# Kernel optimization log

Hardware: AMD Instinct MI355X
Metric: run time of the kernel (lower is better)

The kernel has to match this reference:

```python
import jax, jax.numpy as jnp
import numpy as np

N = 50000
E = 800000
IN_F = 128
HID = 128
OUT_F = 64
MU = 2.0
EPS = 1e-12


def setup_inputs() -> dict:
    key = jax.random.key(0)
    ks = jax.random.split(key, 20)
    d = {}
    d["x"] = jax.random.normal(ks[0], (N, IN_F), dtype=jnp.float32)
    d["edge_src"] = jax.random.randint(ks[1], (E,), 0, N, dtype=jnp.int32)
    d["edge_dst"] = jax.random.randint(ks[2], (E,), 0, N, dtype=jnp.int32)
    d["edge_val"] = jax.random.uniform(ks[3], (E,), dtype=jnp.float32)
    # layer 0: in=128 -> pool=128 -> out=128 (activation=relu)
    s0 = 1.0 / np.sqrt(IN_F)
    d["pool_w0"] = jax.random.uniform(ks[4], (IN_F, IN_F), jnp.float32, -s0, s0)
    d["pool_b0"] = jax.random.uniform(ks[5], (IN_F,), jnp.float32, -s0, s0)
    d["fc1_w0"] = jax.random.uniform(ks[6], (HID, IN_F), jnp.float32, -s0, s0)
    d["fc1_b0"] = jax.random.uniform(ks[7], (HID,), jnp.float32, -s0, s0)
    d["fc2_w0"] = jax.random.uniform(ks[8], (HID, IN_F), jnp.float32, -s0, s0)
    d["fc2_b0"] = jax.random.uniform(ks[9], (HID,), jnp.float32, -s0, s0)
    # layer 1 (final): in=128 -> pool=128 -> out=64 (no activation)
    s1 = 1.0 / np.sqrt(HID)
    d["pool_w1"] = jax.random.uniform(ks[10], (HID, HID), jnp.float32, -s1, s1)
    d["pool_b1"] = jax.random.uniform(ks[11], (HID,), jnp.float32, -s1, s1)
    d["fc1_w1"] = jax.random.uniform(ks[12], (OUT_F, HID), jnp.float32, -s1, s1)
    d["fc1_b1"] = jax.random.uniform(ks[13], (OUT_F,), jnp.float32, -s1, s1)
    d["fc2_w1"] = jax.random.uniform(ks[14], (OUT_F, HID), jnp.float32, -s1, s1)
    d["fc2_b1"] = jax.random.uniform(ks[15], (OUT_F,), jnp.float32, -s1, s1)
    return d


def _sage_conv(x, src, dst, val, pw, pb, w1, b1, w2, b2, act):
    # L2-normalize rows (F.normalize(x, dim=1))
    xn = x / jnp.maximum(jnp.linalg.norm(x, axis=1, keepdims=True), EPS)
    h = jax.nn.relu(xn @ pw.T + pb)               # [N, pool]
    h_mu = h ** MU                                # elementwise pow
    # spmm(adj, h_mu): gather source rows, scale by edge weight, scatter-add to dst rows
    agg = jax.ops.segment_sum(h_mu[src] * val[:, None], dst, num_segments=N)
    agg = agg ** (1.0 / MU)                       # generalized-mean root
    out = (h @ w1.T + b1) + (agg @ w2.T + b2)
    return jax.nn.relu(out) if act else out


def reference(x, edge_src, edge_dst, edge_val,
              pool_w0, pool_b0, fc1_w0, fc1_b0, fc2_w0, fc2_b0,
              pool_w1, pool_b1, fc1_w1, fc1_b1, fc2_w1, fc2_b1):
    h = _sage_conv(x, edge_src, edge_dst, edge_val,
                   pool_w0, pool_b0, fc1_w0, fc1_b0, fc2_w0, fc2_b0, act=True)
    out = _sage_conv(h, edge_src, edge_dst, edge_val,
                     pool_w1, pool_b1, fc1_w1, fc1_b1, fc2_w1, fc2_b1, act=False)
    return out
```

## Files before the change

### kernel.cpp

```cpp
#include <hip/hip_runtime.h>

#define FF 128
#define BCAP 8192
#define CHUNK 4096
#define PITCH 136
#define BSTRIDE 32
#define PBCACHE 6144

typedef __attribute__((ext_vector_type(8))) short short8;
typedef __attribute__((ext_vector_type(4))) float f32x4;

__device__ __forceinline__ unsigned short bf16_rne(float f) {
    unsigned u = __float_as_uint(f);
    u += 0x7fffu + ((u >> 16) & 1u);
    return (unsigned short)(u >> 16);
}
__device__ __forceinline__ float bf16_to_f32(unsigned short h) {
    return __uint_as_float(((unsigned)h) << 16);
}

__global__ __launch_bounds__(256, 2)
void poolpartA_kernel(const float* __restrict__ x,
                      const unsigned short* __restrict__ Wh, const unsigned short* __restrict__ Wl,
                      const float* __restrict__ bias,
                      unsigned short* __restrict__ hout,
                      const int* __restrict__ esrc, const int* __restrict__ edst,
                      const float* __restrict__ eval,
                      int* __restrict__ bucket_cnt, int2* __restrict__ ebuf,
                      int N, int E, int nchunks)
{
    __shared__ alignas(16) char smem[37888];
    const int t = threadIdx.x;

    if (blockIdx.x < nchunks) {
        int* cnt   = (int*)smem;
        int* sc    = cnt + 256;
        int* excl  = sc + 256;
        int* cur   = excl + 256;
        int* gbase = cur + 256;
        int2* staged = (int2*)(smem + 5 * 256 * 4);
        const int e0 = blockIdx.x * CHUNK;
        const int n  = min(CHUNK, E - e0);

        unsigned pk[16]; float vr[16];
        #pragma unroll
        for (int k = 0; k < 16; ++k) {
            const int i = t + k * 256;
            pk[k] = 0xFFFFFFFFu;
            if (i < n) {
                int d = edst[e0 + i];
                int s = esrc[e0 + i];
                pk[k] = (unsigned)((s & 0xffff) | (d << 16));
                vr[k] = eval[e0 + i];
            }
        }

        cnt[t] = 0;
        __syncthreads();
        #pragma unroll
        for (int k = 0; k < 16; ++k)
            if (pk[k] != 0xFFFFFFFFu) atomicAdd(&cnt[pk[k] >> 24], 1);
        __syncthreads();

        sc[t] = cnt[t];
        __syncthreads();
        #pragma unroll
        for (int off = 1; off < 256; off <<= 1) {
            int v = (t >= off) ? sc[t - off] : 0;
            __syncthreads();
            sc[t] += v;
            __syncthreads();
        }
        excl[t] = sc[t] - cnt[t];
        cur[t]  = excl[t];
        if (cnt[t] > 0) gbase[t] = atomicAdd(&bucket_cnt[t * BSTRIDE], cnt[t]);
        __syncthreads();

        #pragma unroll
        for (int k = 0; k < 16; ++k) {
            if (pk[k] != 0xFFFFFFFFu) {
                int b = pk[k] >> 24;
                int slot = atomicAdd(&cur[b], 1);
                staged[slot] = make_int2((int)pk[k], __float_as_int(vr[k]));
            }
        }
        __syncthreads();

        for (int p = t; p < n; p += 256) {
            int2 ent = staged[p];
            int b = ((unsigned)ent.x) >> 24;
            int gpos = gbase[b] + (p - excl[b]);
            ebuf[(size_t)b * BCAP + gpos] = ent;
        }
    } else {
        unsigned short* sX = (unsigned short*)smem;
        float* sNorm = (float*)(smem + 64 * PITCH * 2);
        const int tile = blockIdx.x - nchunks;

        const int lane = t & 63, wave = t >> 6;
        const int quad = lane >> 4, l16 = lane & 15;

        short8 Bh[2][4], Bl[2][4];
        #pragma unroll
        for (int c = 0; c < 2; ++c) {
            const int jt = 2 * wave + c;
            #pragma unroll
            for (int tt = 0; tt < 4; ++tt) {
                const size_t o = ((size_t)(jt * 4 + tt) * 64 + lane) * 8;
                Bh[c][tt] = *(const short8*)&Wh[o];
                Bl[c][tt] = *(const short8*)&Wl[o];
            }
        }

        #pragma unroll
        for (int rg = 0; rg < 2; ++rg) {
            const int row = rg * 32 + (t >> 3);
            const int c0  = (t & 7) * 16;
            const int n   = tile * 64 + row;
            const int base = row * PITCH + c0;
            float v[16];
            if (n < N) {
                const float4* p = (const float4*)(x + (size_t)n * FF + c0);
                #pragma unroll
                for (int i = 0; i < 4; ++i) {
                    float4 q = p[i];
                    v[4*i] = q.x; v[4*i+1] = q.y; v[4*i+2] = q.z; v[4*i+3] = q.w;
                }
            } else {
                #pragma unroll
                for (int i = 0; i < 16; ++i) v[i] = 0.f;
            }
            float ss = 0.f;
            #pragma unroll
            for (int i = 0; i < 16; ++i) ss = fmaf(v[i], v[i], ss);
            union { unsigned short u[8]; short8 s; } h0, h1;
            #pragma unroll
            for (int i = 0; i < 8; ++i) {
                h0.u[i] = bf16_rne(v[i]);
                h1.u[i] = bf16_rne(v[8 + i]);
            }
            *(short8*)&sX[base]     = h0.s;
            *(short8*)&sX[base + 8] = h1.s;
            ss += __shfl_xor(ss, 1);
            ss += __shfl_xor(ss, 2);
            ss += __shfl_xor(ss, 4);
            if ((t & 7) == 0) sNorm[row] = 1.0f / fmaxf(sqrtf(ss), 1e-12f);
        }
        __syncthreads();

        f32x4 acc[4][2];
        #pragma unroll
        for (int r = 0; r < 4; ++r)
            #pragma unroll
            for (int c = 0; c < 2; ++c) {
                f32x4 z = {0.f, 0.f, 0.f, 0.f};
                acc[r][c] = z;
            }

        #pragma unroll
        for (int tt = 0; tt < 4; ++tt) {
            short8 Ah[4];
            #pragma unroll
            for (int r = 0; r < 4; ++r)
                Ah[r] = *(const short8*)&sX[(r * 16 + l16) * PITCH + tt * 32 + quad * 8];
            #pragma unroll
            for (int c = 0; c < 2; ++c)
                #pragma unroll
                for (int r = 0; r < 4; ++r) {
                    acc[r][c] = __builtin_amdgcn_mfma_f32_16x16x32_bf16(Ah[r], Bh[c][tt], acc[r][c], 0, 0, 0);
                    acc[r][c] = __builtin_amdgcn_mfma_f32_16x16x32_bf16(Ah[r], Bl[c][tt], acc[r][c], 0, 0, 0);
                }
        }

        __syncthreads();
        #pragma unroll
        for (int c = 0; c < 2; ++c) {
            const int j = (2 * wave + c) * 16 + l16;
            const float bj = bias[j];
            #pragma unroll
            for (int r = 0; r < 4; ++r) {
                #pragma unroll
                for (int g = 0; g < 4; ++g) {
                    const int nl = r * 16 + quad * 4 + g;
                    float s = sNorm[nl];
                    float val = fmaf(acc[r][c][g], s, bj);
                    val = fmaxf(val, 0.f);
                    sX[nl * PITCH + j] = bf16_rne(val);
                }
            }
        }
        __syncthreads();
        #pragma unroll
        for (int rg = 0; rg < 2; ++rg) {
            const int row = rg * 32 + (t >> 3);
            const int c0  = (t & 7) * 16;
            const int n   = tile * 64 + row;
            if (n < N) {
                const int base = row * PITCH + c0;
                *(short8*)&hout[(size_t)n * FF + c0]     = *(short8*)&sX[base];
                *(short8*)&hout[(size_t)n * FF + c0 + 8] = *(short8*)&sX[base + 8];
            }
        }
    }
}

struct WPack {
    const float* src[6];
    unsigned short* hi[6];
    unsigned short* lo[6];
    int n[6];
};

__global__ __launch_bounds__(256)
void wprep_kernel(WPack p, int* __restrict__ bucket_cnt)
{
    if (blockIdx.x == 0) {
        for (int i = threadIdx.x; i < 256 * BSTRIDE; i += 256) bucket_cnt[i] = 0;
    }
    int id = blockIdx.x * 256 + threadIdx.x;
    #pragma unroll
    for (int i = 0; i < 6; ++i) {
        if (id < p.n[i]) {
            float f = p.src[i][id];
            unsigned short h = bf16_rne(f);
            const int j = id >> 7, k = id & 127;
            const int jt = j >> 4, l16 = j & 15;
            const int t = k >> 5, quad = (k >> 3) & 3, j8 = k & 7;
            const size_t o = ((size_t)((jt * 4 + t) * 4 + quad) * 16 + l16) * 8 + j8;
            p.hi[i][o] = h;
            p.lo[i][o] = bf16_rne(f - bf16_to_f32(h));
            return;
        }
        id -= p.n[i];
    }
}

__global__ __launch_bounds__(256)
void partB_kernel(const int* __restrict__ bucket_cnt, const int2* __restrict__ ebuf,
                  int* __restrict__ offsets, int2* __restrict__ edata,
                  int N, int E, int nbuck)
{
    __shared__ int pre[256], hist[256], sc[256], excl[256], cur[256];
    __shared__ int2 sBuf[PBCACHE];
    const int t = threadIdx.x;
    const int b = blockIdx.x;

    const int cnt_self = bucket_cnt[b * BSTRIDE];
    const int2* ib = ebuf + (size_t)b * BCAP;
    const bool useL = (cnt_self <= PBCACHE);

    if (useL)
        for (int i = t; i < cnt_self; i += 256) sBuf[i] = ib[i];

    pre[t] = (t < nbuck) ? bucket_cnt[t * BSTRIDE] : 0;
    hist[t] = 0;
    __syncthreads();
    #pragma unroll
    for (int off = 1; off < 256; off <<= 1) {
        int v = (t >= off) ? pre[t - off] : 0;
        __syncthreads();
        pre[t] += v;
        __syncthreads();
    }
    const int base = (b == 0) ? 0 : pre[b - 1];
    const int cnt  = cnt_self;

    for (int i = t; i < cnt; i += 256) {
        int2 ent = useL ? sBuf[i] : ib[i];
        atomicAdd(&hist[(((unsigned)ent.x) >> 16) & 255], 1);
    }
    __syncthreads();

    sc[t] = hist[t];
    __syncthreads();
    #pragma unroll
    for (int off = 1; off < 256; off <<= 1) {
        int v = (t >= off) ? sc[t - off] : 0;
        __syncthreads();
        sc[t] += v;
        __syncthreads();
    }
    excl[t] = sc[t] - hist[t];
    cur[t]  = excl[t];

    const int node = b * 256 + t;
    if (node <= N) offsets[node] = base + excl[t];
    __syncthreads();

    for (int i = t; i < cnt; i += 256) {
        int2 ent = useL ? sBuf[i] : ib[i];
        int l = (((unsigned)ent.x) >> 16) & 255;
        int pos = base + atomicAdd(&cur[l], 1);
        edata[pos] = make_int2(ent.x & 0xffff, ent.y);
    }
}

__global__ __launch_bounds__(256)
void agg_kernel(const unsigned short* __restrict__ hp, const int* __restrict__ offsets,
                const int2* __restrict__ edata,
                unsigned short* __restrict__ aggh, int N)
{
    const int w = __builtin_amdgcn_readfirstlane(blockIdx.x * 4 + (threadIdx.x >> 6));
    if (w >= N) return;
    const int lane = threadIdx.x & 63;
    const int fo = lane * 2;

    int e = offsets[w];
    const int end = offsets[w + 1];

    float2 a0 = {0,0}, a1 = {0,0}, a2 = {0,0}, a3 = {0,0};

#define FMA1(A, V, U) { \
        float flo_ = __uint_as_float((U) << 16); \
        float fhi_ = __uint_as_float((U) & 0xffff0000u); \
        A.x = fmaf((V) * flo_, flo_, A.x); \
        A.y = fmaf((V) * fhi_, fhi_, A.y); }

    if ((e & 1) && e < end) {
        int2 ed = edata[e];
        unsigned u = *(const unsigned*)&hp[(size_t)ed.x * FF + fo];
        FMA1(a0, __int_as_float(ed.y), u);
        ++e;
    }
    for (; e + 7 < end; e += 8) {
        int4 p0 = *(const int4*)&edata[e];
        int4 p1 = *(const int4*)&edata[e + 2];
        int4 p2 = *(const int4*)&edata[e + 4];
        int4 p3 = *(const int4*)&edata[e + 6];
        unsigned u0 = *(const unsigned*)&hp[(size_t)p0.x * FF + fo];
        unsigned u1 = *(const unsigned*)&hp[(size_t)p0.z * FF + fo];
        unsigned u2 = *(const unsigned*)&hp[(size_t)p1.x * FF + fo];
        unsigned u3 = *(const unsigned*)&hp[(size_t)p1.z * FF + fo];
        unsigned u4 = *(const unsigned*)&hp[(size_t)p2.x * FF + fo];
        unsigned u5 = *(const unsigned*)&hp[(size_t)p2.z * FF + fo];
        unsigned u6 = *(const unsigned*)&hp[(size_t)p3.x * FF + fo];
        unsigned u7 = *(const unsigned*)&hp[(size_t)p3.z * FF + fo];
        FMA1(a0, __int_as_float(p0.y), u0);
        FMA1(a1, __int_as_float(p0.w), u1);
        FMA1(a2, __int_as_float(p1.y), u2);
        FMA1(a3, __int_as_float(p1.w), u3);
        FMA1(a0, __int_as_float(p2.y), u4);
        FMA1(a1, __int_as_float(p2.w), u5);
        FMA1(a2, __int_as_float(p3.y), u6);
        FMA1(a3, __int_as_float(p3.w), u7);
    }
    if (e + 3 < end) {
        int4 p0 = *(const int4*)&edata[e];
        int4 p1 = *(const int4*)&edata[e + 2];
        unsigned u0 = *(const unsigned*)&hp[(size_t)p0.x * FF + fo];
        unsigned u1 = *(const unsigned*)&hp[(size_t)p0.z * FF + fo];
        unsigned u2 = *(const unsigned*)&hp[(size_t)p1.x * FF + fo];
        unsigned u3 = *(const unsigned*)&hp[(size_t)p1.z * FF + fo];
        FMA1(a0, __int_as_float(p0.y), u0);
        FMA1(a1, __int_as_float(p0.w), u1);
        FMA1(a2, __int_as_float(p1.y), u2);
        FMA1(a3, __int_as_float(p1.w), u3);
        e += 4;
    }
    if (e + 1 < end) {
        int4 p = *(const int4*)&edata[e];
        unsigned u0 = *(const unsigned*)&hp[(size_t)p.x * FF + fo];
        unsigned u1 = *(const unsigned*)&hp[(size_t)p.z * FF + fo];
        FMA1(a0, __int_as_float(p.y), u0);
        FMA1(a1, __int_as_float(p.w), u1);
        e += 2;
    }
    if (e < end) {
        int2 ed = edata[e];
        unsigned u = *(const unsigned*)&hp[(size_t)ed.x * FF + fo];
        FMA1(a0, __int_as_float(ed.y), u);
    }
#undef FMA1

    float rlo = sqrtf(a0.x + a1.x + a2.x + a3.x);
    float rhi = sqrtf(a0.y + a1.y + a2.y + a3.y);
    unsigned outw = (unsigned)bf16_rne(rlo) | ((unsigned)bf16_rne(rhi) << 16);
    *(unsigned*)&aggh[(size_t)w * FF + fo] = outw;
}

__global__ __launch_bounds__(256, 2)
void mm2pool_kernel(const unsigned short* __restrict__ hin,
                    const unsigned short* __restrict__ aggh,
                    const unsigned short* __restrict__ W1h, const unsigned short* __restrict__ W1l,
                    const unsigned short* __restrict__ W2h, const unsigned short* __restrict__ W2l,
                    const float* __restrict__ b1, const float* __restrict__ b2,
                    const unsigned short* __restrict__ PWh, const unsigned short* __restrict__ PWl,
                    const float* __restrict__ pb,
                    unsigned short* __restrict__ hout, int N)
{
    __shared__ unsigned short sH[64 * PITCH];
    __shared__ unsigned short sA[64 * PITCH];
    __shared__ float sNorm[64];

    const int tid  = threadIdx.x;
    const int tile = blockIdx.x;
    const int lane = tid & 63, wave = tid >> 6;
    const int quad = lane >> 4, l16 = lane & 15;

    short8 hreg[2][2], areg[2][2];
    #pragma unroll
    for (int rg = 0; rg < 2; ++rg) {
        const int row = rg * 32 + (tid >> 3);
        const int c0  = (tid & 7) * 16;
        const int n   = tile * 64 + row;
        short8 z = {0,0,0,0,0,0,0,0};
        hreg[rg][0] = z; hreg[rg][1] = z;
        areg[rg][0] = z; areg[rg][1] = z;
        if (n < N) {
            const short8* ph = (const short8*)(hin  + (size_t)n * FF + c0);
            const short8* pa = (const short8*)(aggh + (size_t)n * FF + c0);
            hreg[rg][0] = ph[0]; hreg[rg][1] = ph[1];
            areg[rg][0] = pa[0]; areg[rg][1] = pa[1];
        }
    }

    short8 B1hf[2][4], B1lf[2][4], B2hf[2][4], B2lf[2][4];
    #pragma unroll
    for (int c = 0; c < 2; ++c) {
        const int jt = 2 * wave + c;
        #pragma unroll
        for (int t = 0; t < 4; ++t) {
            const size_t o = ((size_t)(jt * 4 + t) * 64 + lane) * 8;
            B1hf[c][t] = *(const short8*)&W1h[o];
            B1lf[c][t] = *(const short8*)&W1l[o];
            B2hf[c][t] = *(const short8*)&W2h[o];
            B2lf[c][t] = *(const short8*)&W2l[o];
        }
    }

    #pragma unroll
    for (int rg = 0; rg < 2; ++rg) {
        const int row = rg * 32 + (tid >> 3);
        const int base = row * PITCH + (tid & 7) * 16;
        *(short8*)&sH[base]     = hreg[rg][0];
        *(short8*)&sH[base + 8] = hreg[rg][1];
        *(short8*)&sA[base]     = areg[rg][0];
        *(short8*)&sA[base + 8] = areg[rg][1];
    }
    __syncthreads();

    f32x4 acc[4][2];
    #pragma unroll
    for (int r = 0; r < 4; ++r)
        #pragma unroll
        for (int c = 0; c < 2; ++c) {
            f32x4 z = {0.f, 0.f, 0.f, 0.f};
            acc[r][c] = z;
        }

    #pragma unroll
    for (int t = 0; t < 4; ++t) {
        short8 Hf[4], AH[4];
        #pragma unroll
        for (int r = 0; r < 4; ++r) {
            const int off = (r * 16 + l16) * PITCH + t * 32 + quad * 8;
            Hf[r] = *(const short8*)&sH[off];
            AH[r] = *(const short8*)&sA[off];
        }
        #pragma unroll
        for (int c = 0; c < 2; ++c)
            #pragma unroll
            for (int r = 0; r < 4; ++r) {
                acc[r][c] = __builtin_amdgcn_mfma_f32_16x16x32_bf16(Hf[r], B1hf[c][t], acc[r][c], 0, 0, 0);
                acc[r][c] = __builtin_amdgcn_mfma_f32_16x16x32_bf16(Hf[r], B1lf[c][t], acc[r][c], 0, 0, 0);
                acc[r][c] = __builtin_amdgcn_mfma_f32_16x16x32_bf16(AH[r], B2hf[c][t], acc[r][c], 0, 0, 0);
                acc[r][c] = __builtin_amdgcn_mfma_f32_16x16x32_bf16(AH[r], B2lf[c][t], acc[r][c], 0, 0, 0);
            }
    }

    short8 Ph[2][4], Pl[2][4];
    #pragma unroll
    for (int c = 0; c < 2; ++c) {
        const int jt = 2 * wave + c;
        #pragma unroll
        for (int t = 0; t < 4; ++t) {
            const size_t o = ((size_t)(jt * 4 + t) * 64 + lane) * 8;
            Ph[c][t] = *(const short8*)&PWh[o];
            Pl[c][t] = *(const short8*)&PWl[o];
        }
    }

    __syncthreads();

    #pragma unroll
    for (int c = 0; c < 2; ++c) {
        const int j = (2 * wave + c) * 16 + l16;
        const float bj = b1[j] + b2[j];
        #pragma unroll
        for (int r = 0; r < 4; ++r) {
            #pragma unroll
            for (int g = 0; g < 4; ++g) {
                const int nl = r * 16 + quad * 4 + g;
                float val = fmaxf(acc[r][c][g] + bj, 0.f);
                sH[nl * PITCH + j] = bf16_rne(val);
            }
        }
    }
    __syncthreads();

    #pragma unroll
    for (int rg = 0; rg < 2; ++rg) {
        const int row = rg * 32 + (tid >> 3);
        const int c0  = (tid & 7) * 16;
        union { short8 s; unsigned short u[8]; } a, b;
        a.s = *(short8*)&sH[row * PITCH + c0];
        b.s = *(short8*)&sH[row * PITCH + c0 + 8];
        float ss = 0.f;
        #pragma unroll
        for (int i = 0; i < 8; ++i) {
            float fa = bf16_to_f32(a.u[i]);
            float fb = bf16_to_f32(b.u[i]);
            ss = fmaf(fa, fa, fmaf(fb, fb, ss));
        }
        ss += __shfl_xor(ss, 1);
        ss += __shfl_xor(ss, 2);
        ss += __shfl_xor(ss, 4);
        if ((tid & 7) == 0) sNorm[row] = 1.0f / fmaxf(sqrtf(ss), 1e-12f);
    }
    __syncthreads();

    f32x4 acc2[4][2];
    #pragma unroll
    for (int r = 0; r < 4; ++r)
        #pragma unroll
        for (int c = 0; c < 2; ++c) {
            f32x4 z = {0.f, 0.f, 0.f, 0.f};
            acc2[r][c] = z;
        }

    #pragma unroll
    for (int t = 0; t < 4; ++t) {
        short8 Ah[4];
        #pragma unroll
        for (int r = 0; r < 4; ++r)
            Ah[r] = *(const short8*)&sH[(r * 16 + l16) * PITCH + t * 32 + quad * 8];
        #pragma unroll
        for (int c = 0; c < 2; ++c)
            #pragma unroll
            for (int r = 0; r < 4; ++r) {
                acc2[r][c] = __builtin_amdgcn_mfma_f32_16x16x32_bf16(Ah[r], Ph[c][t], acc2[r][c], 0, 0, 0);
                acc2[r][c] = __builtin_amdgcn_mfma_f32_16x16x32_bf16(Ah[r], Pl[c][t], acc2[r][c], 0, 0, 0);
            }
    }

    __syncthreads();
    #pragma unroll
    for (int c = 0; c < 2; ++c) {
        const int j = (2 * wave + c) * 16 + l16;
        const float pbj = pb[j];
        #pragma unroll
        for (int r = 0; r < 4; ++r) {
            #pragma unroll
            for (int g = 0; g < 4; ++g) {
                const int nl = r * 16 + quad * 4 + g;
                float s = sNorm[nl];
                float val = fmaxf(fmaf(acc2[r][c][g], s, pbj), 0.f);
                sA[nl * PITCH + j] = bf16_rne(val);
            }
        }
    }
    __syncthreads();
    #pragma unroll
    for (int rg = 0; rg < 2; ++rg) {
        const int row = rg * 32 + (tid >> 3);
        const int c0  = (tid & 7) * 16;
        const int n   = tile * 64 + row;
        if (n < N) {
            const int base = row * PITCH + c0;
            *(short8*)&hout[(size_t)n * FF + c0]     = *(short8*)&sA[base];
            *(short8*)&hout[(size_t)n * FF + c0 + 8] = *(short8*)&sA[base + 8];
        }
    }
}

#define OPITCH 68
__global__ __launch_bounds__(256, 2)
void mm2_final_kernel(const unsigned short* __restrict__ hin,
                      const unsigned short* __restrict__ aggh,
                      const unsigned short* __restrict__ W1h, const unsigned short* __restrict__ W1l,
                      const unsigned short* __restrict__ W2h, const unsigned short* __restrict__ W2l,
                      const float* __restrict__ b1, const float* __restrict__ b2,
                      float* __restrict__ out, int N)
{
    __shared__ unsigned short sH[64 * PITCH];
    __shared__ unsigned short sA[64 * PITCH];

    const int tid  = threadIdx.x;
    const int tile = blockIdx.x;
    const int lane = tid & 63, wave = tid >> 6;
    const int quad = lane >> 4, l16 = lane & 15;

    short8 hreg[2][2], areg[2][2];
    #pragma unroll
    for (int rg = 0; rg < 2; ++rg) {
        const int row = rg * 32 + (tid >> 3);
        const int c0  = (tid & 7) * 16;
        const int n   = tile * 64 + row;
        short8 z = {0,0,0,0,0,0,0,0};
        hreg[rg][0] = z; hreg[rg][1] = z;
        areg[rg][0] = z; areg[rg][1] = z;
        if (n < N) {
            const short8* ph = (const short8*)(hin  + (size_t)n * FF + c0);
            const short8* pa = (const short8*)(aggh + (size_t)n * FF + c0);
            hreg[rg][0] = ph[0]; hreg[rg][1] = ph[1];
            areg[rg][0] = pa[0]; areg[rg][1] = pa[1];
        }
    }

    short8 B1hf[4], B1lf[4], B2hf[4], B2lf[4];
    #pragma unroll
    for (int t = 0; t < 4; ++t) {
        const size_t o = ((size_t)(wave * 4 + t) * 64 + lane) * 8;
        B1hf[t] = *(const short8*)&W1h[o];
        B1lf[t] = *(const short8*)&W1l[o];
        B2hf[t] = *(const short8*)&W2h[o];
        B2lf[t] = *(const short8*)&W2l[o];
    }

    #pragma unroll
    for (int rg = 0; rg < 2; ++rg) {
        const int row = rg * 32 + (tid >> 3);
        const int base = row * PITCH + (tid & 7) * 16;
        *(short8*)&sH[base]     = hreg[rg][0];
        *(short8*)&sH[base + 8] = hreg[rg][1];
        *(short8*)&sA[base]     = areg[rg][0];
        *(short8*)&sA[base + 8] = areg[rg][1];
    }
    __syncthreads();

    f32x4 acc[4];
    #pragma unroll
    for (int r = 0; r < 4; ++r) {
        f32x4 z = {0.f, 0.f, 0.f, 0.f};
        acc[r] = z;
    }

    #pragma unroll
    for (int t = 0; t < 4; ++t) {
        short8 Hf[4], AH[4];
        #pragma unroll
        for (int r = 0; r < 4; ++r) {
            const int off = (r * 16 + l16) * PITCH + t * 32 + quad * 8;
            Hf[r] = *(const short8*)&sH[off];
            AH[r] = *(const short8*)&sA[off];
        }
        #pragma unroll
        for (int r = 0; r < 4; ++r) {
            acc[r] = __builtin_amdgcn_mfma_f32_16x16x32_bf16(Hf[r], B1hf[t], acc[r], 0, 0, 0);
            acc[r] = __builtin_amdgcn_mfma_f32_16x16x32_bf16(Hf[r], B1lf[t], acc[r], 0, 0, 0);
            acc[r] = __builtin_amdgcn_mfma_f32_16x16x32_bf16(AH[r], B2hf[t], acc[r], 0, 0, 0);
            acc[r] = __builtin_amdgcn_mfma_f32_16x16x32_bf16(AH[r], B2lf[t], acc[r], 0, 0, 0);
        }
    }

    __syncthreads();
    float* sOut = (float*)sH;
    {
        const int j = wave * 16 + l16;
        const float bj = b1[j] + b2[j];
        #pragma unroll
        for (int r = 0; r < 4; ++r) {
            #pragma unroll
            for (int g = 0; g < 4; ++g) {
                const int nl = r * 16 + quad * 4 + g;
                sOut[nl * OPITCH + j] = acc[r][g] + bj;
            }
        }
    }
    __syncthreads();
    {
        const int row = tid >> 2;
        const int seg = tid & 3;
        const int n = tile * 64 + row;
        if (n < N) {
            const float4* src = (const float4*)&sOut[row * OPITCH + seg * 16];
            float4* dst = (float4*)&out[(size_t)n * 64 + seg * 16];
            #pragma unroll
            for (int i = 0; i < 4; ++i) dst[i] = src[i];
        }
    }
}

extern "C" void kernel_launch(void* const* d_in, const int* in_sizes, int n_in,
                              void* d_out, int out_size, void* d_ws, size_t ws_size,
                              hipStream_t stream) {
    const float* x    = (const float*)d_in[0];
    const int*   esrc = (const int*)d_in[1];
    const int*   edst = (const int*)d_in[2];
    const float* eval = (const float*)d_in[3];
    const float* pw0  = (const float*)d_in[4];
    const float* pb0  = (const float*)d_in[5];
    const float* f1w0 = (const float*)d_in[6];
    const float* f1b0 = (const float*)d_in[7];
    const float* f2w0 = (const float*)d_in[8];
    const float* f2b0 = (const float*)d_in[9];
    const float* pw1  = (const float*)d_in[10];
    const float* pb1  = (const float*)d_in[11];
    const float* f1w1 = (const float*)d_in[12];
    const float* f1b1 = (const float*)d_in[13];
    const float* f2w1 = (const float*)d_in[14];
    const float* f2b1 = (const float*)d_in[15];
    float* out = (float*)d_out;

    const int N = in_sizes[0] / FF;
    const int E = in_sizes[1];
    const int nbuck = (N + 255) / 256;

    char* ws = (char*)d_ws;
    const size_t planesz = (size_t)N * FF * 2;
    const size_t A = 256;
    size_t off = 0;
    unsigned short* h    = (unsigned short*)(ws + off); off += (planesz + A - 1) / A * A;
    unsigned short* h2   = (unsigned short*)(ws + off); off += (planesz + A - 1) / A * A;
    unsigned short* aggh = (unsigned short*)(ws + off); off += (planesz + A - 1) / A * A;
    int* offsets = (int*)(ws + off); off += ((size_t)(N + 1) * 4 + A - 1) / A * A;
    int* bucket_cnt = (int*)(ws + off); off += (size_t)256 * BSTRIDE * 4;
    int2* ebuf  = (int2*)(ws + off); off += (size_t)nbuck * BCAP * 8;
    int2* edata = (int2*)(ws + off); off += (size_t)E * 8;
    const int wsz[6] = {128 * FF, 128 * FF, 128 * FF, 128 * FF, 64 * FF, 64 * FF};
    unsigned short* whi[6];
    unsigned short* wlo[6];
    for (int i = 0; i < 6; ++i) {
        whi[i] = (unsigned short*)(ws + off); off += (size_t)wsz[i] * 2;
        wlo[i] = (unsigned short*)(ws + off); off += (size_t)wsz[i] * 2;
    }

    WPack pack;
    const float* wsrc[6] = {pw0, f1w0, f2w0, pw1, f1w1, f2w1};
    int wtotal = 0;
    for (int i = 0; i < 6; ++i) {
        pack.src[i] = wsrc[i]; pack.hi[i] = whi[i]; pack.lo[i] = wlo[i]; pack.n[i] = wsz[i];
        wtotal += wsz[i];
    }

    const int ntiles     = (N + 63) / 64;
    const int nodeblocks = (N + 3) / 4;
    const int nchunks    = (E + CHUNK - 1) / CHUNK;
    dim3 B(256);

    wprep_kernel<<<(wtotal + 255) / 256, B, 0, stream>>>(pack, bucket_cnt);

    poolpartA_kernel<<<nchunks + ntiles, B, 0, stream>>>(
        x, whi[0], wlo[0], pb0, h, esrc, edst, eval, bucket_cnt, ebuf, N, E, nchunks);

    partB_kernel<<<nbuck, B, 0, stream>>>(bucket_cnt, ebuf, offsets, edata, N, E, nbuck);

    agg_kernel<<<nodeblocks, B, 0, stream>>>(h, offsets, edata, aggh, N);

    mm2pool_kernel<<<ntiles, B, 0, stream>>>(
        h, aggh, whi[1], wlo[1], whi[2], wlo[2], f1b0, f2b0,
        whi[3], wlo[3], pb1, h2, N);

    agg_kernel<<<nodeblocks, B, 0, stream>>>(h2, offsets, edata, aggh, N);

    mm2_final_kernel<<<ntiles, B, 0, stream>>>(
        h2, aggh, whi[4], wlo[4], whi[5], wlo[5], f1b1, f2b1, out, N);
}
```

Measured before the change: 217.7 us.

## Split weights into bf16 hi/lo in-kernel and drop weight-prep kernel

```diff
diff --git a/kernel.cpp b/kernel.cpp
--- a/kernel.cpp
+++ b/kernel.cpp
@@ -5,7 +5,6 @@
 #define CHUNK 4096
 #define PITCH 136
 #define BSTRIDE 32
-#define PBCACHE 6144
 
 typedef __attribute__((ext_vector_type(8))) short short8;
 typedef __attribute__((ext_vector_type(4))) float f32x4;
@@ -19,9 +18,24 @@
     return __uint_as_float(((unsigned)h) << 16);
 }
 
+__device__ __forceinline__ void ldwsplit(const float* __restrict__ W, int j, int k,
+                                         short8& hi, short8& lo) {
+    const float4* p = (const float4*)&W[(size_t)j * FF + k];
+    float4 q0 = p[0], q1 = p[1];
+    float f[8] = {q0.x, q0.y, q0.z, q0.w, q1.x, q1.y, q1.z, q1.w};
+    union { unsigned short u[8]; short8 s; } H, L;
+    #pragma unroll
+    for (int i = 0; i < 8; ++i) {
+        unsigned short h = bf16_rne(f[i]);
+        H.u[i] = h;
+        L.u[i] = bf16_rne(f[i] - bf16_to_f32(h));
+    }
+    hi = H.s; lo = L.s;
+}
+
 __global__ __launch_bounds__(256, 2)
 void poolpartA_kernel(const float* __restrict__ x,
-                      const unsigned short* __restrict__ Wh, const unsigned short* __restrict__ Wl,
+                      const float* __restrict__ W,
                       const float* __restrict__ bias,
                       unsigned short* __restrict__ hout,
                       const int* __restrict__ esrc, const int* __restrict__ edst,
@@ -103,13 +117,10 @@
         short8 Bh[2][4], Bl[2][4];
         #pragma unroll
         for (int c = 0; c < 2; ++c) {
-            const int jt = 2 * wave + c;
-            #pragma unroll
-            for (int tt = 0; tt < 4; ++tt) {
-                const size_t o = ((size_t)(jt * 4 + tt) * 64 + lane) * 8;
-                Bh[c][tt] = *(const short8*)&Wh[o];
-                Bl[c][tt] = *(const short8*)&Wl[o];
-            }
+            const int j = (2 * wave + c) * 16 + l16;
+            #pragma unroll
+            for (int tt = 0; tt < 4; ++tt)
+                ldwsplit(W, j, tt * 32 + quad * 8, Bh[c][tt], Bl[c][tt]);
         }
 
         #pragma unroll
@@ -204,54 +215,15 @@
     }
 }
 
-struct WPack {
-    const float* src[6];
-    unsigned short* hi[6];
-    unsigned short* lo[6];
-    int n[6];
-};
-
-__global__ __launch_bounds__(256)
-void wprep_kernel(WPack p, int* __restrict__ bucket_cnt)
-{
-    if (blockIdx.x == 0) {
-        for (int i = threadIdx.x; i < 256 * BSTRIDE; i += 256) bucket_cnt[i] = 0;
-    }
-    int id = blockIdx.x * 256 + threadIdx.x;
-    #pragma unroll
-    for (int i = 0; i < 6; ++i) {
-        if (id < p.n[i]) {
-            float f = p.src[i][id];
-            unsigned short h = bf16_rne(f);
-            const int j = id >> 7, k = id & 127;
-            const int jt = j >> 4, l16 = j & 15;
-            const int t = k >> 5, quad = (k >> 3) & 3, j8 = k & 7;
-            const size_t o = ((size_t)((jt * 4 + t) * 4 + quad) * 16 + l16) * 8 + j8;
-            p.hi[i][o] = h;
-            p.lo[i][o] = bf16_rne(f - bf16_to_f32(h));
-            return;
-        }
-        id -= p.n[i];
-    }
-}
-
 __global__ __launch_bounds__(256)
 void partB_kernel(const int* __restrict__ bucket_cnt, const int2* __restrict__ ebuf,
                   int* __restrict__ offsets, int2* __restrict__ edata,
                   int N, int E, int nbuck)
 {
     __shared__ int pre[256], hist[256], sc[256], excl[256], cur[256];
-    __shared__ int2 sBuf[PBCACHE];
     const int t = threadIdx.x;
     const int b = blockIdx.x;
 
-    const int cnt_self = bucket_cnt[b * BSTRIDE];
-    const int2* ib = ebuf + (size_t)b * BCAP;
-    const bool useL = (cnt_self <= PBCACHE);
-
-    if (useL)
-        for (int i = t; i < cnt_self; i += 256) sBuf[i] = ib[i];
-
     pre[t] = (t < nbuck) ? bucket_cnt[t * BSTRIDE] : 0;
     hist[t] = 0;
     __syncthreads();
@@ -263,12 +235,11 @@
         __syncthreads();
     }
     const int base = (b == 0) ? 0 : pre[b - 1];
-    const int cnt  = cnt_self;
-
-    for (int i = t; i < cnt; i += 256) {
-        int2 ent = useL ? sBuf[i] : ib[i];
-        atomicAdd(&hist[(((unsigned)ent.x) >> 16) & 255], 1);
-    }
+    const int cnt  = pre[b] - base;
+
+    const int2* ib = ebuf + (size_t)b * BCAP;
+    for (int i = t; i < cnt; i += 256)
+        atomicAdd(&hist[(((unsigned)ib[i].x) >> 16) & 255], 1);
     __syncthreads();
 
     sc[t] = hist[t];
@@ -288,7 +259,7 @@
     __syncthreads();
 
     for (int i = t; i < cnt; i += 256) {
-        int2 ent = useL ? sBuf[i] : ib[i];
+        int2 ent = ib[i];
         int l = (((unsigned)ent.x) >> 16) & 255;
         int pos = base + atomicAdd(&cur[l], 1);
         edata[pos] = make_int2(ent.x & 0xffff, ent.y);
@@ -381,11 +352,9 @@
 __global__ __launch_bounds__(256, 2)
 void mm2pool_kernel(const unsigned short* __restrict__ hin,
                     const unsigned short* __restrict__ aggh,
-                    const unsigned short* __restrict__ W1h, const unsigned short* __restrict__ W1l,
-                    const unsigned short* __restrict__ W2h, const unsigned short* __restrict__ W2l,
+                    const float* __restrict__ W1, const float* __restrict__ W2,
                     const float* __restrict__ b1, const float* __restrict__ b2,
-                    const unsigned short* __restrict__ PWh, const unsigned short* __restrict__ PWl,
-                    const float* __restrict__ pb,
+                    const float* __restrict__ PW, const float* __restrict__ pb,
                     unsigned short* __restrict__ hout, int N)
 {
     __shared__ unsigned short sH[64 * PITCH];
@@ -417,14 +386,12 @@
     short8 B1hf[2][4], B1lf[2][4], B2hf[2][4], B2lf[2][4];
     #pragma unroll
     for (int c = 0; c < 2; ++c) {
-        const int jt = 2 * wave + c;
+        const int j = (2 * wave + c) * 16 + l16;
         #pragma unroll
         for (int t = 0; t < 4; ++t) {
-            const size_t o = ((size_t)(jt * 4 + t) * 64 + lane) * 8;
-            B1hf[c][t] = *(const short8*)&W1h[o];
-            B1lf[c][t] = *(const short8*)&W1l[o];
-            B2hf[c][t] = *(const short8*)&W2h[o];
-            B2lf[c][t] = *(const short8*)&W2l[o];
+            const int k = t * 32 + quad * 8;
+            ldwsplit(W1, j, k, B1hf[c][t], B1lf[c][t]);
+            ldwsplit(W2, j, k, B2hf[c][t], B2lf[c][t]);
         }
     }
 
@@ -471,13 +438,10 @@
     short8 Ph[2][4], Pl[2][4];
     #pragma unroll
     for (int c = 0; c < 2; ++c) {
-        const int jt = 2 * wave + c;
-        #pragma unroll
-        for (int t = 0; t < 4; ++t) {
-            const size_t o = ((size_t)(jt * 4 + t) * 64 + lane) * 8;
-            Ph[c][t] = *(const short8*)&PWh[o];
-            Pl[c][t] = *(const short8*)&PWl[o];
-        }
+        const int j = (2 * wave + c) * 16 + l16;
+        #pragma unroll
+        for (int t = 0; t < 4; ++t)
+            ldwsplit(PW, j, t * 32 + quad * 8, Ph[c][t], Pl[c][t]);
     }
 
     __syncthreads();
@@ -577,8 +541,7 @@
 __global__ __launch_bounds__(256, 2)
 void mm2_final_kernel(const unsigned short* __restrict__ hin,
                       const unsigned short* __restrict__ aggh,
-                      const unsigned short* __restrict__ W1h, const unsigned short* __restrict__ W1l,
-                      const unsigned short* __restrict__ W2h, const unsigned short* __restrict__ W2l,
+                      const float* __restrict__ W1, const float* __restrict__ W2,
                       const float* __restrict__ b1, const float* __restrict__ b2,
                       float* __restrict__ out, int N)
 {
@@ -608,13 +571,14 @@
     }
 
     short8 B1hf[4], B1lf[4], B2hf[4], B2lf[4];
-    #pragma unroll
-    for (int t = 0; t < 4; ++t) {
-        const size_t o = ((size_t)(wave * 4 + t) * 64 + lane) * 8;
-        B1hf[t] = *(const short8*)&W1h[o];
-        B1lf[t] = *(const short8*)&W1l[o];
-        B2hf[t] = *(const short8*)&W2h[o];
-        B2lf[t] = *(const short8*)&W2l[o];
+    {
+        const int j = wave * 16 + l16;
+        #pragma unroll
+        for (int t = 0; t < 4; ++t) {
+            const int k = t * 32 + quad * 8;
+            ldwsplit(W1, j, k, B1hf[t], B1lf[t]);
+            ldwsplit(W2, j, k, B2hf[t], B2lf[t]);
+        }
     }
 
     #pragma unroll
@@ -717,42 +681,26 @@
     int* bucket_cnt = (int*)(ws + off); off += (size_t)256 * BSTRIDE * 4;
     int2* ebuf  = (int2*)(ws + off); off += (size_t)nbuck * BCAP * 8;
     int2* edata = (int2*)(ws + off); off += (size_t)E * 8;
-    const int wsz[6] = {128 * FF, 128 * FF, 128 * FF, 128 * FF, 64 * FF, 64 * FF};
-    unsigned short* whi[6];
-    unsigned short* wlo[6];
-    for (int i = 0; i < 6; ++i) {
-        whi[i] = (unsigned short*)(ws + off); off += (size_t)wsz[i] * 2;
-        wlo[i] = (unsigned short*)(ws + off); off += (size_t)wsz[i] * 2;
-    }
-
-    WPack pack;
-    const float* wsrc[6] = {pw0, f1w0, f2w0, pw1, f1w1, f2w1};
-    int wtotal = 0;
-    for (int i = 0; i < 6; ++i) {
-        pack.src[i] = wsrc[i]; pack.hi[i] = whi[i]; pack.lo[i] = wlo[i]; pack.n[i] = wsz[i];
-        wtotal += wsz[i];
-    }
 
     const int ntiles     = (N + 63) / 64;
     const int nodeblocks = (N + 3) / 4;
     const int nchunks    = (E + CHUNK - 1) / CHUNK;
     dim3 B(256);
 
-    wprep_kernel<<<(wtotal + 255) / 256, B, 0, stream>>>(pack, bucket_cnt);
+    hipMemsetAsync(bucket_cnt, 0, (size_t)256 * BSTRIDE * 4, stream);
 
     poolpartA_kernel<<<nchunks + ntiles, B, 0, stream>>>(
-        x, whi[0], wlo[0], pb0, h, esrc, edst, eval, bucket_cnt, ebuf, N, E, nchunks);
+        x, pw0, pb0, h, esrc, edst, eval, bucket_cnt, ebuf, N, E, nchunks);
 
     partB_kernel<<<nbuck, B, 0, stream>>>(bucket_cnt, ebuf, offsets, edata, N, E, nbuck);
 
     agg_kernel<<<nodeblocks, B, 0, stream>>>(h, offsets, edata, aggh, N);
 
     mm2pool_kernel<<<ntiles, B, 0, stream>>>(
-        h, aggh, whi[1], wlo[1], whi[2], wlo[2], f1b0, f2b0,
-        whi[3], wlo[3], pb1, h2, N);
+        h, aggh, f1w0, f2w0, f1b0, f2b0, pw1, pb1, h2, N);
 
     agg_kernel<<<nodeblocks, B, 0, stream>>>(h2, offsets, edata, aggh, N);
 
     mm2_final_kernel<<<ntiles, B, 0, stream>>>(
-        h2, aggh, whi[4], wlo[4], whi[5], wlo[5], f1b1, f2b1, out, N);
-}
+        h2, aggh, f1w1, f2w1, f1b1, f2b1, out, N);
+}
```

Result: slower. 236.3 us (+8.5%).
